# Optimization experiments

Measured on AMD Instinct MI355X. Metric: run time of the kernel, lower is better.

Reference implementation:

```python
import jax, jax.numpy as jnp
import numpy as np

NUM_HEADS = 16  # from init_kwargs


def setup_inputs() -> dict:
    key = jax.random.key(0)
    k1, k2, k3, k4, k5 = jax.random.split(key, 5)
    B, N, C = 2, 2048, 1024
    return {
        "query": jax.random.normal(k1, (B, N, C), dtype=jnp.float32),
        "key": jax.random.normal(k2, (B, N, C), dtype=jnp.float32),
        "value": jax.random.normal(k3, (B, N, C), dtype=jnp.float32),
        "W_merge": jax.random.normal(k4, (C, C), dtype=jnp.float32) * (1.0 / np.sqrt(C)),
        "b_merge": jax.random.normal(k5, (C,), dtype=jnp.float32) * 0.02,
    }


def reference(query, key, value, W_merge, b_merge):
    B, N, C = query.shape
    H = NUM_HEADS
    dim = C // H
    # Faithful to torch: plain reshape (B,N,C) -> (B, dim, H, N), no transpose.
    q = query.reshape(B, dim, H, -1)
    k = key.reshape(B, dim, H, -1)
    v = value.reshape(B, dim, H, -1)
    # Faithful scale: divide by sqrt(N) (sequence length), as in the source.
    scale = 1.0 / np.sqrt(N).astype(np.float32)
    scores = jnp.einsum('bdhn,bdhm->bhnm', q, k) * scale  # [B,H,N,N]
    attn = jax.nn.softmax(scores, axis=-1)
    x = jnp.einsum('bhnm,bdhm->bdhn', attn, v)  # [B,dim,H,N]
    x = x.reshape(B, C, -1)  # [B,C,N]
    # Conv1d(C,C,kernel_size=1) == pointwise channel matmul + bias
    out = jnp.einsum('oc,bcn->bon', W_merge, x) + b_merge[None, :, None]
    return out  # [B,C,N]
```

## Files before the change

kernel.cpp:

```cpp
#include <hip/hip_runtime.h>


#define H 16
#define DIM 64
#define NSEQ 2048
#define CCH 1024
#define BATCH 2
#define DSTR (H * NSEQ)

typedef __attribute__((ext_vector_type(8))) short bf16x8;
typedef __attribute__((ext_vector_type(4))) float f32x4;
typedef __attribute__((ext_vector_type(16))) float f32x16;
typedef __attribute__((ext_vector_type(4))) unsigned int uint32x4;

__device__ __forceinline__ unsigned short f2bf(float x) {
  unsigned int u = __builtin_bit_cast(unsigned int, x);
  u += 0x7FFFu + ((u >> 16) & 1u);
  return (unsigned short)(u >> 16);
}

__device__ __forceinline__ unsigned int pack2bf(float a, float b) {
#if __has_builtin(__builtin_amdgcn_cvt_pk_bf16_f32)
  typedef __attribute__((ext_vector_type(2))) __bf16 bf16x2_t;
  bf16x2_t r = __builtin_amdgcn_cvt_pk_bf16_f32(a, b);
  return __builtin_bit_cast(unsigned int, r);
#else
  unsigned int ua = __builtin_bit_cast(unsigned int, a);
  unsigned int ub = __builtin_bit_cast(unsigned int, b);
  ua += 0x7FFFu + ((ua >> 16) & 1u);
  ub += 0x7FFFu + ((ub >> 16) & 1u);
  return __builtin_amdgcn_perm(ub, ua, 0x07060302u);
#endif
}

__device__ __forceinline__ float fast_exp2(float x) {
#if __has_builtin(__builtin_amdgcn_exp2f)
  return __builtin_amdgcn_exp2f(x);
#else
  return exp2f(x);
#endif
}

__device__ __forceinline__ void permswap32(unsigned int& a, unsigned int& b) {
#if __has_builtin(__builtin_amdgcn_permlane32_swap)
  typedef __attribute__((ext_vector_type(2))) unsigned int uint2v;
  uint2v r = __builtin_amdgcn_permlane32_swap(a, b, false, false);
  a = r[0];
  b = r[1];
#else
  unsigned int ax = (unsigned int)__shfl_xor((int)a, 32, 64);
  unsigned int bx = (unsigned int)__shfl_xor((int)b, 32, 64);
  bool lo = (threadIdx.x & 63) < 32;
  unsigned int na = lo ? a : bx;
  unsigned int nb = lo ? ax : b;
  a = na;
  b = nb;
#endif
}

__device__ __forceinline__ void gld16(const void* g, void* l) {
  __builtin_amdgcn_global_load_lds(
      (const __attribute__((address_space(1))) unsigned int*)g,
      (__attribute__((address_space(3))) unsigned int*)l, 16, 0, 0);
}

__device__ __forceinline__ f32x16 zero16() {
  f32x16 v;
#pragma unroll
  for (int i = 0; i < 16; ++i) v[i] = 0.f;
  return v;
}

__global__ __launch_bounds__(256) void prep_w(const float* __restrict__ W,
                                              unsigned short* __restrict__ Wp) {
  int idx = blockIdx.x * 256 + threadIdx.x;
  int o = idx >> 10, cp = idx & 1023;
  int hh = cp >> 6, d = cp & 63;
  Wp[idx] = f2bf(W[o * CCH + d * H + hh]);
}

__global__ __launch_bounds__(256) void conv_v(const float* __restrict__ v,
                                              unsigned short* __restrict__ Vb) {
  int idx = blockIdx.x * 256 + threadIdx.x;
  float4 x = ((const float4*)v)[idx];
  ushort4 o;
  o.x = f2bf(x.x); o.y = f2bf(x.y); o.z = f2bf(x.z); o.w = f2bf(x.w);
  ((ushort4*)Vb)[idx] = o;
}

__global__ __launch_bounds__(256) void prep_tr(const float* __restrict__ q,
                                               const float* __restrict__ k,
                                               unsigned short* __restrict__ Qt,
                                               unsigned short* __restrict__ Kt) {
  __shared__ unsigned short T[64][72];
  const int tid = threadIdx.x;
  const int n0 = blockIdx.x * 64;
  const int hh = blockIdx.y;
  const int b = blockIdx.z >> 1, t = blockIdx.z & 1;
  const float* src = t ? k : q;
  unsigned short* dst = t ? Kt : Qt;
  const float scl = t ? 1.0f : (0.022097086912079608f * 1.4426950408889634f);
  const size_t base = (size_t)b * (CCH * NSEQ) + (size_t)hh * NSEQ;
#pragma unroll
  for (int it = 0; it < 4; ++it) {
    int i4 = it * 256 + tid;
    int d = i4 >> 4;
    int nn = (i4 & 15) << 2;
    float4 val = *(const float4*)(src + base + (size_t)d * DSTR + n0 + nn);
    T[nn + 0][d] = f2bf(val.x * scl);
    T[nn + 1][d] = f2bf(val.y * scl);
    T[nn + 2][d] = f2bf(val.z * scl);
    T[nn + 3][d] = f2bf(val.w * scl);
  }
  __syncthreads();
  const size_t obase = ((size_t)(b * H + hh) * NSEQ + n0) * 64;
#pragma unroll
  for (int it = 0; it < 2; ++it) {
    int idx = it * 256 + tid;
    int row = idx >> 3, cb = idx & 7;
    *(bf16x8*)(dst + obase + (size_t)row * 64 + cb * 8) = *(const bf16x8*)&T[row][cb * 8];
  }
}

__global__ __launch_bounds__(512, 2) void attn4(const unsigned short* __restrict__ Qt,
                                                const unsigned short* __restrict__ Kt,
                                                const unsigned short* __restrict__ Vb,
                                                unsigned short* __restrict__ xt) {
  __shared__ __align__(16) unsigned char sbuf[65536 + 2048];
  unsigned short* KV = (unsigned short*)sbuf;
  float* lsumLDS = (float*)(sbuf + 65536);
  float* Oex = (float*)sbuf;

  const int tid = threadIdx.x;
  const int w = tid >> 6, lane = tid & 63;
  const int lane31 = lane & 31, hl = lane >> 5;
  const int g = w >> 2, nw = w & 3;
  const int n0 = blockIdx.x * 256;
  const int hh = blockIdx.y, b = blockIdx.z;

  const unsigned short* Qbase = Qt + ((size_t)(b * H + hh) * NSEQ + n0) * 64;
  const unsigned short* Kg = Kt + ((size_t)(b * H + hh) * NSEQ + g * 1024) * 64;
  const unsigned short* Vg = Vb + (size_t)b * (CCH * NSEQ) + (size_t)hh * NSEQ + g * 1024;

  const int r8 = lane >> 3, scb = lane & 7;

#pragma unroll
  for (int i = 0; i < 4; ++i) {
    int row = i * 64 + w * 8 + r8;
    int cbl = scb ^ (row & 7);
    gld16(Qbase + (size_t)row * 64 + cbl * 8, KV + (i * 64 + w * 8) * 64);
  }
  __syncthreads();

  bf16x8 bQ[2][4];
#pragma unroll
  for (int nt = 0; nt < 2; ++nt)
#pragma unroll
    for (int ks = 0; ks < 4; ++ks) {
      int row = nw * 64 + nt * 32 + lane31;
      int phys = (ks * 2 + hl) ^ (row & 7);
      bQ[nt][ks] = *(const bf16x8*)(KV + (size_t)row * 64 + phys * 8);
    }
  __syncthreads();

#define KVOFF(gg, bb, kk) ((((gg)*2 + (bb)) * 2 + (kk)) * 4096)

#pragma unroll
  for (int i = 0; i < 2; ++i) {
    int row = i * 32 + nw * 8 + r8;
    int cbl = scb ^ (row & 7);
    gld16(Kg + (size_t)row * 64 + cbl * 8, KV + KVOFF(g, 0, 0) + (i * 32 + nw * 8) * 64);
    gld16(Vg + (size_t)row * DSTR + cbl * 8, KV + KVOFF(g, 0, 1) + (i * 32 + nw * 8) * 64);
  }
  __syncthreads();

  f32x16 O[2][2];
#pragma unroll
  for (int nt = 0; nt < 2; ++nt)
#pragma unroll
    for (int dt = 0; dt < 2; ++dt) O[nt][dt] = zero16();
  float lsum[2] = {0.f, 0.f};

  for (int it = 0; it < 16; ++it) {
    const int cur = it & 1;
    if (it < 15) {
      const int nxt = cur ^ 1;
      const int m0n = (it + 1) * 64;
#pragma unroll
      for (int i = 0; i < 2; ++i) {
        int row = i * 32 + nw * 8 + r8;
        int cbl = scb ^ (row & 7);
        gld16(Kg + (size_t)(m0n + row) * 64 + cbl * 8,
              KV + KVOFF(g, nxt, 0) + (i * 32 + nw * 8) * 64);
        gld16(Vg + (size_t)row * DSTR + m0n + cbl * 8,
              KV + KVOFF(g, nxt, 1) + (i * 32 + nw * 8) * 64);
      }
    }

#pragma unroll
    for (int mt = 0; mt < 2; ++mt) {
      f32x16 St[2];
      St[0] = zero16();
      St[1] = zero16();
#pragma unroll
      for (int ks = 0; ks < 4; ++ks) {
        int row = mt * 32 + lane31;
        int phys = (ks * 2 + hl) ^ (row & 7);
        bf16x8 aK = *(const bf16x8*)(KV + KVOFF(g, cur, 0) + row * 64 + phys * 8);
        St[0] = __builtin_amdgcn_mfma_f32_32x32x16_bf16(aK, bQ[0][ks], St[0], 0, 0, 0);
        St[1] = __builtin_amdgcn_mfma_f32_32x32x16_bf16(aK, bQ[1][ks], St[1], 0, 0, 0);
      }

      unsigned int pd[2][8];
#pragma unroll
      for (int nt = 0; nt < 2; ++nt)
#pragma unroll
        for (int t = 0; t < 8; ++t) {
          float e0 = fast_exp2(St[nt][2 * t]);
          float e1 = fast_exp2(St[nt][2 * t + 1]);
          lsum[nt] += e0 + e1;
          pd[nt][t] = pack2bf(e0, e1);
        }

      unsigned int s[2][2][4];
#pragma unroll
      for (int nt = 0; nt < 2; ++nt) {
        s[nt][0][0] = pd[nt][0]; s[nt][0][2] = pd[nt][2];
        s[nt][0][1] = pd[nt][1]; s[nt][0][3] = pd[nt][3];
        s[nt][1][0] = pd[nt][4]; s[nt][1][2] = pd[nt][6];
        s[nt][1][1] = pd[nt][5]; s[nt][1][3] = pd[nt][7];
        permswap32(s[nt][0][0], s[nt][0][2]);
        permswap32(s[nt][0][1], s[nt][0][3]);
        permswap32(s[nt][1][0], s[nt][1][2]);
        permswap32(s[nt][1][1], s[nt][1][3]);
      }

#pragma unroll
      for (int ms = 0; ms < 2; ++ms) {
        bf16x8 bV[2];
#pragma unroll
        for (int dt = 0; dt < 2; ++dt) {
          int row = dt * 32 + lane31;
          int phys = (mt * 4 + ms * 2 + hl) ^ (row & 7);
          bV[dt] = *(const bf16x8*)(KV + KVOFF(g, cur, 1) + row * 64 + phys * 8);
        }
#pragma unroll
        for (int nt = 0; nt < 2; ++nt) {
          bf16x8 aP = __builtin_bit_cast(
              bf16x8, (uint32x4){s[nt][ms][0], s[nt][ms][1], s[nt][ms][2], s[nt][ms][3]});
          O[nt][0] = __builtin_amdgcn_mfma_f32_32x32x16_bf16(aP, bV[0], O[nt][0], 0, 0, 0);
          O[nt][1] = __builtin_amdgcn_mfma_f32_32x32x16_bf16(aP, bV[1], O[nt][1], 0, 0, 0);
        }
      }
    }
    __syncthreads();
  }

#pragma unroll
  for (int nt = 0; nt < 2; ++nt) lsum[nt] += __shfl_xor(lsum[nt], 32, 64);
  if (hl == 0) {
#pragma unroll
    for (int nt = 0; nt < 2; ++nt)
      lsumLDS[g * 256 + nw * 64 + nt * 32 + lane31] = lsum[nt];
  }
  if (g == 1) {
#pragma unroll
    for (int nt = 0; nt < 2; ++nt)
#pragma unroll
      for (int dt = 0; dt < 2; ++dt)
#pragma unroll
        for (int r = 0; r < 16; ++r) {
          int nl = nw * 64 + nt * 32 + (r & 3) + 8 * (r >> 2) + 4 * hl;
          Oex[nl * 64 + dt * 32 + lane31] = O[nt][dt][r];
        }
  }
  __syncthreads();
  if (g == 0) {
    const size_t xb = (size_t)b * ((size_t)NSEQ * CCH);
#pragma unroll
    for (int nt = 0; nt < 2; ++nt)
#pragma unroll
      for (int rq = 0; rq < 4; ++rq) {
        int nlb = nw * 64 + nt * 32 + rq * 8 + 4 * hl;
        float4 l0 = *(const float4*)&lsumLDS[nlb];
        float4 l1 = *(const float4*)&lsumLDS[256 + nlb];
        float inv0 = 1.0f / (l0.x + l1.x);
        float inv1 = 1.0f / (l0.y + l1.y);
        float inv2 = 1.0f / (l0.z + l1.z);
        float inv3 = 1.0f / (l0.w + l1.w);
#pragma unroll
        for (int dt = 0; dt < 2; ++dt) {
          int d = dt * 32 + lane31;
#pragma unroll
          for (int rr = 0; rr < 4; ++rr) {
            int r = rq * 4 + rr;
            float val = O[nt][dt][r] + Oex[(nlb + rr) * 64 + d];
            float inv = (rr == 0) ? inv0 : (rr == 1) ? inv1 : (rr == 2) ? inv2 : inv3;
            int n = n0 + nlb + rr;
            xt[xb + (size_t)n * CCH + hh * 64 + d] = f2bf(val * inv);
          }
        }
      }
  }
#undef KVOFF
}

__global__ __launch_bounds__(256, 2) void merge3(const unsigned short* __restrict__ Wp,
                                                 const unsigned short* __restrict__ xt,
                                                 const float* __restrict__ bias,
                                                 float* __restrict__ out) {
  __shared__ unsigned short At[2][128 * 64];
  __shared__ unsigned short Bt[2][128 * 64];
  const int tid = threadIdx.x;
  const int w = tid >> 6, lane = tid & 63;
  const int quad = lane >> 4, l16 = lane & 15;
  const int wx = w & 1, wy = w >> 1;
  const int n0 = blockIdx.x * 128, o0 = blockIdx.y * 128, b = blockIdx.z;
  const int srow = w * 8 + (lane >> 3), scb = lane & 7;
  const unsigned short* Bbase = xt + (size_t)b * ((size_t)NSEQ * CCH);

  f32x4 acc[4][4];
#pragma unroll
  for (int ot = 0; ot < 4; ++ot)
#pragma unroll
    for (int nt = 0; nt < 4; ++nt) acc[ot][nt] = (f32x4){0.f, 0.f, 0.f, 0.f};

#pragma unroll
  for (int i = 0; i < 4; ++i) {
    int row = i * 32 + srow;
    int cbl = scb ^ (row & 7);
    gld16(Wp + (size_t)(o0 + row) * CCH + cbl * 8, &At[0][(i * 32 + w * 8) * 64]);
    gld16(Bbase + (size_t)(n0 + row) * CCH + cbl * 8, &Bt[0][(i * 32 + w * 8) * 64]);
  }
  __syncthreads();

  for (int it = 0; it < 16; ++it) {
    const int cur = it & 1;
    if (it < 15) {
      const int nxt = cur ^ 1;
      const int c0 = (it + 1) * 64;
#pragma unroll
      for (int i = 0; i < 4; ++i) {
        int row = i * 32 + srow;
        int cbl = scb ^ (row & 7);
        gld16(Wp + (size_t)(o0 + row) * CCH + c0 + cbl * 8, &At[nxt][(i * 32 + w * 8) * 64]);
        gld16(Bbase + (size_t)(n0 + row) * CCH + c0 + cbl * 8, &Bt[nxt][(i * 32 + w * 8) * 64]);
      }
    }
#pragma unroll
    for (int ks = 0; ks < 2; ++ks) {
      bf16x8 aW[4], bX[4];
      int phys = ((ks * 4 + quad) ^ (l16 & 7)) * 8;
#pragma unroll
      for (int t = 0; t < 4; ++t) {
        aW[t] = *(const bf16x8*)&At[cur][(wy * 64 + t * 16 + l16) * 64 + phys];
        bX[t] = *(const bf16x8*)&Bt[cur][(wx * 64 + t * 16 + l16) * 64 + phys];
      }
#pragma unroll
      for (int ot = 0; ot < 4; ++ot)
#pragma unroll
        for (int nt = 0; nt < 4; ++nt)
          acc[ot][nt] =
              __builtin_amdgcn_mfma_f32_16x16x32_bf16(aW[ot], bX[nt], acc[ot][nt], 0, 0, 0);
    }
    __syncthreads();
  }

#pragma unroll
  for (int ot = 0; ot < 4; ++ot)
#pragma unroll
    for (int r = 0; r < 4; ++r) {
      int o = o0 + wy * 64 + ot * 16 + quad * 4 + r;
      float bi = bias[o];
#pragma unroll
      for (int nt = 0; nt < 4; ++nt)
        out[(size_t)b * ((size_t)CCH * NSEQ) + (size_t)o * NSEQ + n0 + wx * 64 + nt * 16 + l16] =
            acc[ot][nt][r] + bi;
    }
}

extern "C" void kernel_launch(void* const* d_in, const int* in_sizes, int n_in,
                              void* d_out, int out_size, void* d_ws, size_t ws_size,
                              hipStream_t stream) {
  const float* q = (const float*)d_in[0];
  const float* k = (const float*)d_in[1];
  const float* v = (const float*)d_in[2];
  const float* W = (const float*)d_in[3];
  const float* bias = (const float*)d_in[4];
  float* out = (float*)d_out;

  unsigned short* Wp = (unsigned short*)d_ws;
  unsigned short* xt = Wp + (1u << 20);
  unsigned short* Qt = xt + (4u << 20);
  unsigned short* Kt = Qt + (4u << 20);
  unsigned short* Vb = Kt + (4u << 20);

  hipLaunchKernelGGL(prep_w, dim3(4096), dim3(256), 0, stream, W, Wp);
  hipLaunchKernelGGL(conv_v, dim3(4096), dim3(256), 0, stream, v, Vb);
  hipLaunchKernelGGL(prep_tr, dim3(NSEQ / 64, H, BATCH * 2), dim3(256), 0, stream,
                     q, k, Qt, Kt);
  hipLaunchKernelGGL(attn4, dim3(NSEQ / 256, H, BATCH), dim3(512), 0, stream,
                     Qt, Kt, Vb, xt);
  hipLaunchKernelGGL(merge3, dim3(NSEQ / 128, CCH / 128, BATCH), dim3(256), 0, stream,
                     Wp, xt, bias, out);
}
```

Baseline: 177.9 us.

## Fuse prep kernels, simplify attention to single-group waves, shrink merge tiles

```diff
diff --git a/kernel.cpp b/kernel.cpp
--- a/kernel.cpp
+++ b/kernel.cpp
@@ -2,7 +2,6 @@
 
 
 #define H 16
-#define DIM 64
 #define NSEQ 2048
 #define CCH 1024
 #define BATCH 2
@@ -71,169 +70,158 @@
   return v;
 }
 
-__global__ __launch_bounds__(256) void prep_w(const float* __restrict__ W,
-                                              unsigned short* __restrict__ Wp) {
-  int idx = blockIdx.x * 256 + threadIdx.x;
-  int o = idx >> 10, cp = idx & 1023;
-  int hh = cp >> 6, d = cp & 63;
-  Wp[idx] = f2bf(W[o * CCH + d * H + hh]);
-}
-
-__global__ __launch_bounds__(256) void conv_v(const float* __restrict__ v,
-                                              unsigned short* __restrict__ Vb) {
-  int idx = blockIdx.x * 256 + threadIdx.x;
-  float4 x = ((const float4*)v)[idx];
-  ushort4 o;
-  o.x = f2bf(x.x); o.y = f2bf(x.y); o.z = f2bf(x.z); o.w = f2bf(x.w);
-  ((ushort4*)Vb)[idx] = o;
-}
-
-__global__ __launch_bounds__(256) void prep_tr(const float* __restrict__ q,
-                                               const float* __restrict__ k,
-                                               unsigned short* __restrict__ Qt,
-                                               unsigned short* __restrict__ Kt) {
+__global__ __launch_bounds__(256) void prep_all(const float* __restrict__ W,
+                                                const float* __restrict__ v,
+                                                const float* __restrict__ q,
+                                                const float* __restrict__ k,
+                                                unsigned short* __restrict__ Wp,
+                                                unsigned short* __restrict__ Vb,
+                                                unsigned short* __restrict__ Qt,
+                                                unsigned short* __restrict__ Kt) {
   __shared__ unsigned short T[64][72];
-  const int tid = threadIdx.x;
-  const int n0 = blockIdx.x * 64;
-  const int hh = blockIdx.y;
-  const int b = blockIdx.z >> 1, t = blockIdx.z & 1;
-  const float* src = t ? k : q;
-  unsigned short* dst = t ? Kt : Qt;
-  const float scl = t ? 1.0f : (0.022097086912079608f * 1.4426950408889634f);
-  const size_t base = (size_t)b * (CCH * NSEQ) + (size_t)hh * NSEQ;
-#pragma unroll
-  for (int it = 0; it < 4; ++it) {
-    int i4 = it * 256 + tid;
-    int d = i4 >> 4;
-    int nn = (i4 & 15) << 2;
-    float4 val = *(const float4*)(src + base + (size_t)d * DSTR + n0 + nn);
-    T[nn + 0][d] = f2bf(val.x * scl);
-    T[nn + 1][d] = f2bf(val.y * scl);
-    T[nn + 2][d] = f2bf(val.z * scl);
-    T[nn + 3][d] = f2bf(val.w * scl);
-  }
-  __syncthreads();
-  const size_t obase = ((size_t)(b * H + hh) * NSEQ + n0) * 64;
-#pragma unroll
-  for (int it = 0; it < 2; ++it) {
-    int idx = it * 256 + tid;
-    int row = idx >> 3, cb = idx & 7;
-    *(bf16x8*)(dst + obase + (size_t)row * 64 + cb * 8) = *(const bf16x8*)&T[row][cb * 8];
-  }
-}
-
-__global__ __launch_bounds__(512, 2) void attn4(const unsigned short* __restrict__ Qt,
-                                                const unsigned short* __restrict__ Kt,
-                                                const unsigned short* __restrict__ Vb,
-                                                unsigned short* __restrict__ xt) {
-  __shared__ __align__(16) unsigned char sbuf[65536 + 2048];
-  unsigned short* KV = (unsigned short*)sbuf;
-  float* lsumLDS = (float*)(sbuf + 65536);
-  float* Oex = (float*)sbuf;
+  const int bid = blockIdx.x, tid = threadIdx.x;
+
+  if (bid < 1024) {
+    const int o = bid;
+    const int cp = tid * 4;
+    const int hh = cp >> 6;
+    const int d0 = cp & 63;
+    const float* Wr = W + (size_t)o * CCH;
+    ushort4 ov;
+    ov.x = f2bf(Wr[(d0 + 0) * H + hh]);
+    ov.y = f2bf(Wr[(d0 + 1) * H + hh]);
+    ov.z = f2bf(Wr[(d0 + 2) * H + hh]);
+    ov.w = f2bf(Wr[(d0 + 3) * H + hh]);
+    *(ushort4*)&Wp[(size_t)o * CCH + cp] = ov;
+  } else if (bid < 5120) {
+    int idx = (bid - 1024) * 256 + tid;
+    float4 x = ((const float4*)v)[idx];
+    ushort4 o;
+    o.x = f2bf(x.x); o.y = f2bf(x.y); o.z = f2bf(x.z); o.w = f2bf(x.w);
+    ((ushort4*)Vb)[idx] = o;
+  } else {
+    const int lbid = bid - 5120;
+    const int n0 = (lbid & 31) * 64;
+    const int hh = (lbid >> 5) & 15;
+    const int zz = lbid >> 9;
+    const int b = zz >> 1, t = zz & 1;
+    const float* src = t ? k : q;
+    unsigned short* dst = t ? Kt : Qt;
+    const float scl = t ? 1.0f : (0.022097086912079608f * 1.4426950408889634f);
+    const size_t base = (size_t)b * (CCH * NSEQ) + (size_t)hh * NSEQ;
+#pragma unroll
+    for (int it = 0; it < 4; ++it) {
+      int i4 = it * 256 + tid;
+      int d = i4 >> 4;
+      int nn = (i4 & 15) << 2;
+      float4 val = *(const float4*)(src + base + (size_t)d * DSTR + n0 + nn);
+      T[nn + 0][d] = f2bf(val.x * scl);
+      T[nn + 1][d] = f2bf(val.y * scl);
+      T[nn + 2][d] = f2bf(val.z * scl);
+      T[nn + 3][d] = f2bf(val.w * scl);
+    }
+    __syncthreads();
+    const size_t obase = ((size_t)(b * H + hh) * NSEQ + n0) * 64;
+#pragma unroll
+    for (int it = 0; it < 2; ++it) {
+      int idx = it * 256 + tid;
+      int row = idx >> 3, cb = idx & 7;
+      *(bf16x8*)(dst + obase + (size_t)row * 64 + cb * 8) = *(const bf16x8*)&T[row][cb * 8];
+    }
+  }
+}
+
+__global__ __launch_bounds__(256) void attn5(const unsigned short* __restrict__ Qt,
+                                             const unsigned short* __restrict__ Kt,
+                                             const unsigned short* __restrict__ Vb,
+                                             unsigned short* __restrict__ xt) {
+  __shared__ __align__(16) unsigned short S[4 * 4096];
+#define KS(bb) (S + (bb) * 8192)
+#define VS(bb) (S + (bb) * 8192 + 4096)
 
   const int tid = threadIdx.x;
   const int w = tid >> 6, lane = tid & 63;
   const int lane31 = lane & 31, hl = lane >> 5;
-  const int g = w >> 2, nw = w & 3;
-  const int n0 = blockIdx.x * 256;
+  const int n0 = blockIdx.x * 128;
   const int hh = blockIdx.y, b = blockIdx.z;
 
   const unsigned short* Qbase = Qt + ((size_t)(b * H + hh) * NSEQ + n0) * 64;
-  const unsigned short* Kg = Kt + ((size_t)(b * H + hh) * NSEQ + g * 1024) * 64;
-  const unsigned short* Vg = Vb + (size_t)b * (CCH * NSEQ) + (size_t)hh * NSEQ + g * 1024;
+  const unsigned short* Kbase = Kt + ((size_t)(b * H + hh) * NSEQ) * 64;
+  const unsigned short* Vbase = Vb + (size_t)b * (CCH * NSEQ) + (size_t)hh * NSEQ;
 
   const int r8 = lane >> 3, scb = lane & 7;
 
 #pragma unroll
   for (int i = 0; i < 4; ++i) {
-    int row = i * 64 + w * 8 + r8;
+    int row = i * 32 + w * 8 + r8;
     int cbl = scb ^ (row & 7);
-    gld16(Qbase + (size_t)row * 64 + cbl * 8, KV + (i * 64 + w * 8) * 64);
+    gld16(Qbase + (size_t)row * 64 + cbl * 8, S + (i * 32 + w * 8) * 64);
   }
   __syncthreads();
 
-  bf16x8 bQ[2][4];
-#pragma unroll
-  for (int nt = 0; nt < 2; ++nt)
-#pragma unroll
-    for (int ks = 0; ks < 4; ++ks) {
-      int row = nw * 64 + nt * 32 + lane31;
-      int phys = (ks * 2 + hl) ^ (row & 7);
-      bQ[nt][ks] = *(const bf16x8*)(KV + (size_t)row * 64 + phys * 8);
-    }
+  bf16x8 bQ[4];
+#pragma unroll
+  for (int ks = 0; ks < 4; ++ks) {
+    int row = w * 32 + lane31;
+    int phys = (ks * 2 + hl) ^ (row & 7);
+    bQ[ks] = *(const bf16x8*)(S + (size_t)row * 64 + phys * 8);
+  }
   __syncthreads();
 
-#define KVOFF(gg, bb, kk) ((((gg)*2 + (bb)) * 2 + (kk)) * 4096)
-
 #pragma unroll
   for (int i = 0; i < 2; ++i) {
-    int row = i * 32 + nw * 8 + r8;
+    int row = i * 32 + w * 8 + r8;
     int cbl = scb ^ (row & 7);
-    gld16(Kg + (size_t)row * 64 + cbl * 8, KV + KVOFF(g, 0, 0) + (i * 32 + nw * 8) * 64);
-    gld16(Vg + (size_t)row * DSTR + cbl * 8, KV + KVOFF(g, 0, 1) + (i * 32 + nw * 8) * 64);
+    gld16(Kbase + (size_t)row * 64 + cbl * 8, KS(0) + (i * 32 + w * 8) * 64);
+    gld16(Vbase + (size_t)row * DSTR + cbl * 8, VS(0) + (i * 32 + w * 8) * 64);
   }
   __syncthreads();
 
-  f32x16 O[2][2];
-#pragma unroll
-  for (int nt = 0; nt < 2; ++nt)
-#pragma unroll
-    for (int dt = 0; dt < 2; ++dt) O[nt][dt] = zero16();
-  float lsum[2] = {0.f, 0.f};
-
-  for (int it = 0; it < 16; ++it) {
+  f32x16 O[2];
+  O[0] = zero16();
+  O[1] = zero16();
+  float lsum = 0.f;
+
+  for (int it = 0; it < 32; ++it) {
     const int cur = it & 1;
-    if (it < 15) {
+    if (it < 31) {
       const int nxt = cur ^ 1;
       const int m0n = (it + 1) * 64;
 #pragma unroll
       for (int i = 0; i < 2; ++i) {
-        int row = i * 32 + nw * 8 + r8;
+        int row = i * 32 + w * 8 + r8;
         int cbl = scb ^ (row & 7);
-        gld16(Kg + (size_t)(m0n + row) * 64 + cbl * 8,
-              KV + KVOFF(g, nxt, 0) + (i * 32 + nw * 8) * 64);
-        gld16(Vg + (size_t)row * DSTR + m0n + cbl * 8,
-              KV + KVOFF(g, nxt, 1) + (i * 32 + nw * 8) * 64);
+        gld16(Kbase + (size_t)(m0n + row) * 64 + cbl * 8, KS(nxt) + (i * 32 + w * 8) * 64);
+        gld16(Vbase + (size_t)row * DSTR + m0n + cbl * 8, VS(nxt) + (i * 32 + w * 8) * 64);
       }
     }
 
 #pragma unroll
     for (int mt = 0; mt < 2; ++mt) {
-      f32x16 St[2];
-      St[0] = zero16();
-      St[1] = zero16();
+      f32x16 St = zero16();
 #pragma unroll
       for (int ks = 0; ks < 4; ++ks) {
         int row = mt * 32 + lane31;
         int phys = (ks * 2 + hl) ^ (row & 7);
-        bf16x8 aK = *(const bf16x8*)(KV + KVOFF(g, cur, 0) + row * 64 + phys * 8);
-        St[0] = __builtin_amdgcn_mfma_f32_32x32x16_bf16(aK, bQ[0][ks], St[0], 0, 0, 0);
-        St[1] = __builtin_amdgcn_mfma_f32_32x32x16_bf16(aK, bQ[1][ks], St[1], 0, 0, 0);
-      }
-
-      unsigned int pd[2][8];
-#pragma unroll
-      for (int nt = 0; nt < 2; ++nt)
-#pragma unroll
-        for (int t = 0; t < 8; ++t) {
-          float e0 = fast_exp2(St[nt][2 * t]);
-          float e1 = fast_exp2(St[nt][2 * t + 1]);
-          lsum[nt] += e0 + e1;
-          pd[nt][t] = pack2bf(e0, e1);
-        }
-
-      unsigned int s[2][2][4];
-#pragma unroll
-      for (int nt = 0; nt < 2; ++nt) {
-        s[nt][0][0] = pd[nt][0]; s[nt][0][2] = pd[nt][2];
-        s[nt][0][1] = pd[nt][1]; s[nt][0][3] = pd[nt][3];
-        s[nt][1][0] = pd[nt][4]; s[nt][1][2] = pd[nt][6];
-        s[nt][1][1] = pd[nt][5]; s[nt][1][3] = pd[nt][7];
-        permswap32(s[nt][0][0], s[nt][0][2]);
-        permswap32(s[nt][0][1], s[nt][0][3]);
-        permswap32(s[nt][1][0], s[nt][1][2]);
-        permswap32(s[nt][1][1], s[nt][1][3]);
-      }
+        bf16x8 aK = *(const bf16x8*)(KS(cur) + row * 64 + phys * 8);
+        St = __builtin_amdgcn_mfma_f32_32x32x16_bf16(aK, bQ[ks], St, 0, 0, 0);
+      }
+
+      unsigned int pd[8];
+#pragma unroll
+      for (int t = 0; t < 8; ++t) {
+        float e0 = fast_exp2(St[2 * t]);
+        float e1 = fast_exp2(St[2 * t + 1]);
+        lsum += e0 + e1;
+        pd[t] = pack2bf(e0, e1);
+      }
+
+      unsigned int s0[4] = {pd[0], pd[1], pd[2], pd[3]};
+      unsigned int s1[4] = {pd[4], pd[5], pd[6], pd[7]};
+      permswap32(s0[0], s0[2]);
+      permswap32(s0[1], s0[3]);
+      permswap32(s1[0], s1[2]);
+      permswap32(s1[1], s1[3]);
 
 #pragma unroll
       for (int ms = 0; ms < 2; ++ms) {
@@ -242,94 +230,63 @@
         for (int dt = 0; dt < 2; ++dt) {
           int row = dt * 32 + lane31;
           int phys = (mt * 4 + ms * 2 + hl) ^ (row & 7);
-          bV[dt] = *(const bf16x8*)(KV + KVOFF(g, cur, 1) + row * 64 + phys * 8);
+          bV[dt] = *(const bf16x8*)(VS(cur) + row * 64 + phys * 8);
         }
-#pragma unroll
-        for (int nt = 0; nt < 2; ++nt) {
-          bf16x8 aP = __builtin_bit_cast(
-              bf16x8, (uint32x4){s[nt][ms][0], s[nt][ms][1], s[nt][ms][2], s[nt][ms][3]});
-          O[nt][0] = __builtin_amdgcn_mfma_f32_32x32x16_bf16(aP, bV[0], O[nt][0], 0, 0, 0);
-          O[nt][1] = __builtin_amdgcn_mfma_f32_32x32x16_bf16(aP, bV[1], O[nt][1], 0, 0, 0);
-        }
+        const unsigned int* sp = ms ? s1 : s0;
+        bf16x8 aP = __builtin_bit_cast(bf16x8, (uint32x4){sp[0], sp[1], sp[2], sp[3]});
+        O[0] = __builtin_amdgcn_mfma_f32_32x32x16_bf16(aP, bV[0], O[0], 0, 0, 0);
+        O[1] = __builtin_amdgcn_mfma_f32_32x32x16_bf16(aP, bV[1], O[1], 0, 0, 0);
       }
     }
     __syncthreads();
   }
 
-#pragma unroll
-  for (int nt = 0; nt < 2; ++nt) lsum[nt] += __shfl_xor(lsum[nt], 32, 64);
-  if (hl == 0) {
-#pragma unroll
-    for (int nt = 0; nt < 2; ++nt)
-      lsumLDS[g * 256 + nw * 64 + nt * 32 + lane31] = lsum[nt];
-  }
-  if (g == 1) {
-#pragma unroll
-    for (int nt = 0; nt < 2; ++nt)
-#pragma unroll
-      for (int dt = 0; dt < 2; ++dt)
-#pragma unroll
-        for (int r = 0; r < 16; ++r) {
-          int nl = nw * 64 + nt * 32 + (r & 3) + 8 * (r >> 2) + 4 * hl;
-          Oex[nl * 64 + dt * 32 + lane31] = O[nt][dt][r];
-        }
-  }
-  __syncthreads();
-  if (g == 0) {
-    const size_t xb = (size_t)b * ((size_t)NSEQ * CCH);
-#pragma unroll
-    for (int nt = 0; nt < 2; ++nt)
-#pragma unroll
-      for (int rq = 0; rq < 4; ++rq) {
-        int nlb = nw * 64 + nt * 32 + rq * 8 + 4 * hl;
-        float4 l0 = *(const float4*)&lsumLDS[nlb];
-        float4 l1 = *(const float4*)&lsumLDS[256 + nlb];
-        float inv0 = 1.0f / (l0.x + l1.x);
-        float inv1 = 1.0f / (l0.y + l1.y);
-        float inv2 = 1.0f / (l0.z + l1.z);
-        float inv3 = 1.0f / (l0.w + l1.w);
-#pragma unroll
-        for (int dt = 0; dt < 2; ++dt) {
-          int d = dt * 32 + lane31;
-#pragma unroll
-          for (int rr = 0; rr < 4; ++rr) {
-            int r = rq * 4 + rr;
-            float val = O[nt][dt][r] + Oex[(nlb + rr) * 64 + d];
-            float inv = (rr == 0) ? inv0 : (rr == 1) ? inv1 : (rr == 2) ? inv2 : inv3;
-            int n = n0 + nlb + rr;
-            xt[xb + (size_t)n * CCH + hh * 64 + d] = f2bf(val * inv);
-          }
-        }
-      }
-  }
-#undef KVOFF
-}
-
-__global__ __launch_bounds__(256, 2) void merge3(const unsigned short* __restrict__ Wp,
-                                                 const unsigned short* __restrict__ xt,
-                                                 const float* __restrict__ bias,
-                                                 float* __restrict__ out) {
-  __shared__ unsigned short At[2][128 * 64];
+  lsum += __shfl_xor(lsum, 32, 64);
+  float linv = 1.0f / lsum;
+
+  const size_t xb = (size_t)b * ((size_t)NSEQ * CCH);
+#pragma unroll
+  for (int r = 0; r < 16; ++r) {
+    int nl = (r & 3) + 8 * (r >> 2) + 4 * hl;
+    float inv = __shfl(linv, nl, 64);
+    int n = n0 + w * 32 + nl;
+    size_t rowb = xb + (size_t)n * CCH + hh * 64;
+    xt[rowb + lane31] = f2bf(O[0][r] * inv);
+    xt[rowb + 32 + lane31] = f2bf(O[1][r] * inv);
+  }
+#undef KS
+#undef VS
+}
+
+__global__ __launch_bounds__(256) void merge4(const unsigned short* __restrict__ Wp,
+                                              const unsigned short* __restrict__ xt,
+                                              const float* __restrict__ bias,
+                                              float* __restrict__ out) {
+  __shared__ unsigned short At[2][64 * 64];
   __shared__ unsigned short Bt[2][128 * 64];
   const int tid = threadIdx.x;
   const int w = tid >> 6, lane = tid & 63;
   const int quad = lane >> 4, l16 = lane & 15;
-  const int wx = w & 1, wy = w >> 1;
-  const int n0 = blockIdx.x * 128, o0 = blockIdx.y * 128, b = blockIdx.z;
+  const int n0 = blockIdx.x * 128, o0 = blockIdx.y * 64, b = blockIdx.z;
   const int srow = w * 8 + (lane >> 3), scb = lane & 7;
   const unsigned short* Bbase = xt + (size_t)b * ((size_t)NSEQ * CCH);
 
-  f32x4 acc[4][4];
+  f32x4 acc[4][2];
 #pragma unroll
   for (int ot = 0; ot < 4; ++ot)
 #pragma unroll
-    for (int nt = 0; nt < 4; ++nt) acc[ot][nt] = (f32x4){0.f, 0.f, 0.f, 0.f};
-
+    for (int nt = 0; nt < 2; ++nt) acc[ot][nt] = (f32x4){0.f, 0.f, 0.f, 0.f};
+
+#pragma unroll
+  for (int i = 0; i < 2; ++i) {
+    int row = i * 32 + srow;
+    int cbl = scb ^ (row & 7);
+    gld16(Wp + (size_t)(o0 + row) * CCH + cbl * 8, &At[0][(i * 32 + w * 8) * 64]);
+  }
 #pragma unroll
   for (int i = 0; i < 4; ++i) {
     int row = i * 32 + srow;
     int cbl = scb ^ (row & 7);
-    gld16(Wp + (size_t)(o0 + row) * CCH + cbl * 8, &At[0][(i * 32 + w * 8) * 64]);
     gld16(Bbase + (size_t)(n0 + row) * CCH + cbl * 8, &Bt[0][(i * 32 + w * 8) * 64]);
   }
   __syncthreads();
@@ -340,26 +297,32 @@
       const int nxt = cur ^ 1;
       const int c0 = (it + 1) * 64;
 #pragma unroll
+      for (int i = 0; i < 2; ++i) {
+        int row = i * 32 + srow;
+        int cbl = scb ^ (row & 7);
+        gld16(Wp + (size_t)(o0 + row) * CCH + c0 + cbl * 8, &At[nxt][(i * 32 + w * 8) * 64]);
+      }
+#pragma unroll
       for (int i = 0; i < 4; ++i) {
         int row = i * 32 + srow;
         int cbl = scb ^ (row & 7);
-        gld16(Wp + (size_t)(o0 + row) * CCH + c0 + cbl * 8, &At[nxt][(i * 32 + w * 8) * 64]);
         gld16(Bbase + (size_t)(n0 + row) * CCH + c0 + cbl * 8, &Bt[nxt][(i * 32 + w * 8) * 64]);
       }
     }
 #pragma unroll
     for (int ks = 0; ks < 2; ++ks) {
-      bf16x8 aW[4], bX[4];
       int phys = ((ks * 4 + quad) ^ (l16 & 7)) * 8;
-#pragma unroll
-      for (int t = 0; t < 4; ++t) {
-        aW[t] = *(const bf16x8*)&At[cur][(wy * 64 + t * 16 + l16) * 64 + phys];
-        bX[t] = *(const bf16x8*)&Bt[cur][(wx * 64 + t * 16 + l16) * 64 + phys];
-      }
+      bf16x8 aW[4], bX[2];
 #pragma unroll
       for (int ot = 0; ot < 4; ++ot)
-#pragma unroll
-        for (int nt = 0; nt < 4; ++nt)
+        aW[ot] = *(const bf16x8*)&At[cur][(ot * 16 + l16) * 64 + phys];
+#pragma unroll
+      for (int nt = 0; nt < 2; ++nt)
+        bX[nt] = *(const bf16x8*)&Bt[cur][(w * 32 + nt * 16 + l16) * 64 + phys];
+#pragma unroll
+      for (int ot = 0; ot < 4; ++ot)
+#pragma unroll
+        for (int nt = 0; nt < 2; ++nt)
           acc[ot][nt] =
               __builtin_amdgcn_mfma_f32_16x16x32_bf16(aW[ot], bX[nt], acc[ot][nt], 0, 0, 0);
     }
@@ -367,16 +330,18 @@
   }
 
 #pragma unroll
-  for (int ot = 0; ot < 4; ++ot)
+  for (int ot = 0; ot < 4; ++ot) {
+    float4 bi = *(const float4*)&bias[o0 + ot * 16 + quad * 4];
 #pragma unroll
     for (int r = 0; r < 4; ++r) {
-      int o = o0 + wy * 64 + ot * 16 + quad * 4 + r;
-      float bi = bias[o];
-#pragma unroll
-      for (int nt = 0; nt < 4; ++nt)
-        out[(size_t)b * ((size_t)CCH * NSEQ) + (size_t)o * NSEQ + n0 + wx * 64 + nt * 16 + l16] =
-            acc[ot][nt][r] + bi;
-    }
+      int o = o0 + ot * 16 + quad * 4 + r;
+      float br = (r == 0) ? bi.x : (r == 1) ? bi.y : (r == 2) ? bi.z : bi.w;
+#pragma unroll
+      for (int nt = 0; nt < 2; ++nt)
+        out[(size_t)b * ((size_t)CCH * NSEQ) + (size_t)o * NSEQ + n0 + w * 32 + nt * 16 + l16] =
+            acc[ot][nt][r] + br;
+    }
+  }
 }
 
 extern "C" void kernel_launch(void* const* d_in, const int* in_sizes, int n_in,
@@ -395,12 +360,8 @@
   unsigned short* Kt = Qt + (4u << 20);
   unsigned short* Vb = Kt + (4u << 20);
 
-  hipLaunchKernelGGL(prep_w, dim3(4096), dim3(256), 0, stream, W, Wp);
-  hipLaunchKernelGGL(conv_v, dim3(4096), dim3(256), 0, stream, v, Vb);
-  hipLaunchKernelGGL(prep_tr, dim3(NSEQ / 64, H, BATCH * 2), dim3(256), 0, stream,
-                     q, k, Qt, Kt);
-  hipLaunchKernelGGL(attn4, dim3(NSEQ / 256, H, BATCH), dim3(512), 0, stream,
-                     Qt, Kt, Vb, xt);
-  hipLaunchKernelGGL(merge3, dim3(NSEQ / 128, CCH / 128, BATCH), dim3(256), 0, stream,
+  hipLaunchKernelGGL(prep_all, dim3(7168), dim3(256), 0, stream, W, v, q, k, Wp, Vb, Qt, Kt);
+  hipLaunchKernelGGL(attn5, dim3(NSEQ / 128, H, BATCH), dim3(256), 0, stream, Qt, Kt, Vb, xt);
+  hipLaunchKernelGGL(merge4, dim3(NSEQ / 128, CCH / 64, BATCH), dim3(256), 0, stream,
                      Wp, xt, bias, out);
 }
```

Measured after the change: 171.5 us. 1.04x faster.
